# Kernel tuning notes

Hardware: AMD Instinct MI355X
Metric: run time of the kernel (lower is better)

## Reference

```python
import jax, jax.numpy as jnp
import numpy as np

DIM = 768
NUM_HEADS = 12
HEAD_DIM = DIM // NUM_HEADS
SCALE = HEAD_DIM ** (-0.5)


def setup_inputs() -> dict:
    key = jax.random.key(0)
    ks = jax.random.split(key, 8)
    B, Nq, Nk, Nv = 2, 2048, 2048, 2048
    init = 0.02
    return {
        "xq": jax.random.normal(ks[0], (B, Nq, DIM), dtype=jnp.float32),
        "xk": jax.random.normal(ks[1], (B, Nk, DIM), dtype=jnp.float32),
        "xv": jax.random.normal(ks[2], (B, Nv, DIM), dtype=jnp.float32),
        # torch nn.Linear weights are [out_features, in_features]; qkv_bias=False
        "Wq": jax.random.normal(ks[3], (DIM, DIM), dtype=jnp.float32) * init,
        "Wk": jax.random.normal(ks[4], (DIM, DIM), dtype=jnp.float32) * init,
        "Wv": jax.random.normal(ks[5], (DIM, DIM), dtype=jnp.float32) * init,
        "Wp": jax.random.normal(ks[6], (DIM, DIM), dtype=jnp.float32) * init,
        "bp": jax.random.normal(ks[7], (DIM,), dtype=jnp.float32) * init,
    }


def reference(xq, xk, xv, Wq, Wk, Wv, Wp, bp):
    B, Nq, C = xq.shape
    H, D = NUM_HEADS, HEAD_DIM
    # linear projections (torch Linear: x @ W.T), split heads -> [B, H, N, D]
    q = (xq @ Wq.T).reshape(B, Nq, H, D).transpose(0, 2, 1, 3)
    k = (xk @ Wk.T).reshape(B, xk.shape[1], H, D).transpose(0, 2, 1, 3)
    v = (xv @ Wv.T).reshape(B, xv.shape[1], H, D).transpose(0, 2, 1, 3)
    # attention scores [B, H, Nq, Nk]
    attn = jnp.einsum("bhqd,bhkd->bhqk", q, k) * SCALE
    attn = jax.nn.softmax(attn, axis=-1)
    # weighted values -> merge heads [B, Nq, C]
    out = jnp.einsum("bhqk,bhkd->bhqd", attn, v)
    out = out.transpose(0, 2, 1, 3).reshape(B, Nq, C)
    return out @ Wp.T + bp
```

## Files before the change

### kernel.cpp

```cpp
#include <hip/hip_runtime.h>
#include <hip/hip_bf16.h>


#define NSEQ 2048
#define CDIM 768
#define NH   12
#define HD   64
#define MTOT 4096
#define XEL  (MTOT*CDIM)
#define WEL  (CDIM*CDIM)
#define X8   (XEL/8)
#define W8   (WEL/8)
#define PSTR 72
#define QSCALE 0.18033688011112042f

typedef __attribute__((ext_vector_type(8))) short bf16x8;
typedef __attribute__((ext_vector_type(4))) float floatx4;

static __device__ __forceinline__ unsigned short f2bf(float f) {
  union { float f; unsigned int u; } v; v.f = f;
  return (unsigned short)((v.u + 0x8000u) >> 16);
}
static __device__ __forceinline__ unsigned pk2bf(float a, float b) {
  unsigned ua = __float_as_uint(a) + 0x8000u;
  unsigned ub = __float_as_uint(b) + 0x8000u;
  return __builtin_amdgcn_perm(ub, ua, 0x07060302);
}

static __device__ __forceinline__ void lds16(const void* g, void* l) {
  __builtin_amdgcn_global_load_lds(
      (const __attribute__((address_space(1))) unsigned int*)g,
      (__attribute__((address_space(3))) unsigned int*)l, 16, 0, 0);
}

__global__ __launch_bounds__(256) void cast_all(
    const float* __restrict__ xq, const float* __restrict__ xk,
    const float* __restrict__ xv, const float* __restrict__ wq,
    const float* __restrict__ wk, const float* __restrict__ wv,
    const float* __restrict__ wp,
    unsigned short* __restrict__ Xq, unsigned short* __restrict__ Xk,
    unsigned short* __restrict__ Xv, unsigned short* __restrict__ Wq,
    unsigned short* __restrict__ Wk, unsigned short* __restrict__ Wv,
    unsigned short* __restrict__ Wp) {
  int i = blockIdx.x * 256 + threadIdx.x;
  const float* s; unsigned short* d; int off;
  if (i < 3 * X8) {
    int t = i / X8; off = i - t * X8;
    s = (t == 0) ? xq : (t == 1) ? xk : xv;
    d = (t == 0) ? Xq : (t == 1) ? Xk : Xv;
  } else {
    int j = i - 3 * X8; int t = j / W8; off = j - t * W8;
    s = (t == 0) ? wq : (t == 1) ? wk : (t == 2) ? wv : wp;
    d = (t == 0) ? Wq : (t == 1) ? Wk : (t == 2) ? Wv : Wp;
  }
  const float4* sp = (const float4*)s + (size_t)off * 2;
  float4 a = sp[0], b = sp[1];
  uint4 o;
  o.x = pk2bf(a.x, a.y); o.y = pk2bf(a.z, a.w);
  o.z = pk2bf(b.x, b.y); o.w = pk2bf(b.z, b.w);
  *(uint4*)(d + (size_t)off * 8) = o;
}

__global__ __launch_bounds__(256) void gemm_qkv(
    const unsigned short* __restrict__ Xq, const unsigned short* __restrict__ Xk,
    const unsigned short* __restrict__ Xv, const unsigned short* __restrict__ Wq,
    const unsigned short* __restrict__ Wk, const unsigned short* __restrict__ Wv,
    unsigned short* __restrict__ Qo, unsigned short* __restrict__ Ko,
    unsigned short* __restrict__ Vo) {
  int z = blockIdx.z;
  const unsigned short* A; const unsigned short* B; int m0, n0;
  if (z == 0)      { A = Xq; B = Wq; m0 = blockIdx.y * 128; n0 = blockIdx.x * 128; }
  else if (z == 1) { A = Xk; B = Wk; m0 = blockIdx.y * 128; n0 = blockIdx.x * 128; }
  else             { A = Wv; B = Xv; m0 = blockIdx.x * 128; n0 = blockIdx.y * 128; }
  __shared__ __align__(16) unsigned short As[128 * 64];
  __shared__ __align__(16) unsigned short Bs[128 * 64];
  int tid = threadIdx.x, lane = tid & 63, wave = tid >> 6;
  int quad = lane >> 4, l15 = lane & 15, l7 = l15 & 7;
  int wm = (wave >> 1) * 64, wn = (wave & 1) * 64;
  floatx4 acc[4][4];
#pragma unroll
  for (int i = 0; i < 4; i++)
#pragma unroll
    for (int j = 0; j < 4; j++) acc[i][j] = (floatx4){0.f, 0.f, 0.f, 0.f};

  for (int k0 = 0; k0 < CDIM; k0 += 64) {
#pragma unroll
    for (int i = 0; i < 4; i++) {
      int idx = i * 256 + tid;
      int R = idx >> 3, c = (idx & 7) ^ (R & 7);
      lds16(A + (size_t)(m0 + R) * CDIM + k0 + c * 8, &As[idx * 8]);
      lds16(B + (size_t)(n0 + R) * CDIM + k0 + c * 8, &Bs[idx * 8]);
    }
    __syncthreads();
#pragma unroll
    for (int ks = 0; ks < 2; ks++) {
      int csw = ((ks * 4 + quad) ^ l7) * 8;
      bf16x8 af[4], bfr[4];
#pragma unroll
      for (int i = 0; i < 4; i++)
        af[i] = *(const bf16x8*)&As[(wm + i * 16 + l15) * 64 + csw];
#pragma unroll
      for (int i = 0; i < 4; i++)
        bfr[i] = *(const bf16x8*)&Bs[(wn + i * 16 + l15) * 64 + csw];
#pragma unroll
      for (int mi = 0; mi < 4; mi++)
#pragma unroll
        for (int ni = 0; ni < 4; ni++)
          acc[mi][ni] = __builtin_amdgcn_mfma_f32_16x16x32_bf16(
              af[mi], bfr[ni], acc[mi][ni], 0, 0, 0);
    }
    __syncthreads();
  }
#pragma unroll
  for (int mi = 0; mi < 4; mi++) {
#pragma unroll
    for (int ni = 0; ni < 4; ni++) {
#pragma unroll
      for (int r = 0; r < 4; r++) {
        int grow = m0 + wm + mi * 16 + quad * 4 + r;
        int gcol = n0 + wn + ni * 16 + l15;
        float v = acc[mi][ni][r];
        if (z == 0) {
          int b = grow >> 11, nq = grow & 2047, h = gcol >> 6, d = gcol & 63;
          Qo[((size_t)(b * NH + h) * NSEQ + nq) * HD + d] = f2bf(v * QSCALE);
        } else if (z == 1) {
          int b = grow >> 11, nq = grow & 2047, h = gcol >> 6, d = gcol & 63;
          Ko[((size_t)(b * NH + h) * NSEQ + nq) * HD + d] = f2bf(v);
        } else {
          int b = gcol >> 11, nq = gcol & 2047;
          Vo[((size_t)b * CDIM + grow) * NSEQ + nq] = f2bf(v);
        }
      }
    }
  }
}

__global__ __launch_bounds__(128) void attn_kernel(
    const unsigned short* __restrict__ Q, const unsigned short* __restrict__ K,
    const unsigned short* __restrict__ Vt, unsigned short* __restrict__ ctx) {
  int qt = blockIdx.x, bh = blockIdx.y;
  int tid = threadIdx.x, lane = tid & 63, wave = tid >> 6;
  int quad = lane >> 4, l15 = lane & 15, l7 = l15 & 7;
  __shared__ __align__(16) unsigned short Ks[2][64 * 64];
  __shared__ __align__(16) unsigned short Vs[2][64 * 64];
  __shared__ __align__(16) unsigned short Ps[2][32 * PSTR];

  const unsigned short* Qg = Q + ((size_t)bh * NSEQ + qt * 64 + wave * 32) * HD;
  const unsigned short* Kg = K + (size_t)bh * NSEQ * HD;
  const unsigned short* Vg = Vt + (size_t)bh * HD * NSEQ;

  bf16x8 qf[2][2];
#pragma unroll
  for (int qi = 0; qi < 2; qi++)
#pragma unroll
    for (int ks = 0; ks < 2; ks++)
      qf[qi][ks] = *(const bf16x8*)(Qg + (qi * 16 + l15) * HD + ks * 32 + quad * 8);

  int kgo[4], vgo[4], ldst[4];
#pragma unroll
  for (int i = 0; i < 4; i++) {
    int idx = i * 128 + tid;
    int R = idx >> 3, c = (idx & 7) ^ (R & 7);
    kgo[i] = R * HD + c * 8;
    vgo[i] = R * NSEQ + c * 8;
    ldst[i] = idx * 8;
  }
  unsigned short* Pw = &Ps[wave][0];

  float lacc[2] = {0.f, 0.f};
  floatx4 o[2][4];
#pragma unroll
  for (int qi = 0; qi < 2; qi++)
#pragma unroll
    for (int dt = 0; dt < 4; dt++) o[qi][dt] = (floatx4){0.f, 0.f, 0.f, 0.f};

  for (int tt = 0; tt < 16; tt++) {
    int k0 = tt * 128;
#pragma unroll
    for (int h = 0; h < 2; h++) {
      const unsigned short* Kh = Kg + (size_t)(k0 + h * 64) * HD;
      const unsigned short* Vh = Vg + k0 + h * 64;
#pragma unroll
      for (int i = 0; i < 4; i++) {
        lds16(Kh + kgo[i], &Ks[h][ldst[i]]);
        lds16(Vh + vgo[i], &Vs[h][ldst[i]]);
      }
    }
    __syncthreads();
#pragma unroll
    for (int h = 0; h < 2; h++) {
#pragma unroll
      for (int nt = 0; nt < 4; nt++) {
        bf16x8 kf0 = *(const bf16x8*)&Ks[h][(nt * 16 + l15) * 64 + ((quad) ^ l7) * 8];
        bf16x8 kf1 = *(const bf16x8*)&Ks[h][(nt * 16 + l15) * 64 + ((4 + quad) ^ l7) * 8];
#pragma unroll
        for (int qi = 0; qi < 2; qi++) {
          floatx4 st = (floatx4){0.f, 0.f, 0.f, 0.f};
          st = __builtin_amdgcn_mfma_f32_16x16x32_bf16(kf0, qf[qi][0], st, 0, 0, 0);
          st = __builtin_amdgcn_mfma_f32_16x16x32_bf16(kf1, qf[qi][1], st, 0, 0, 0);
          float p0 = __builtin_exp2f(st[0]), p1 = __builtin_exp2f(st[1]);
          float p2 = __builtin_exp2f(st[2]), p3 = __builtin_exp2f(st[3]);
          lacc[qi] += (p0 + p1) + (p2 + p3);
          *(uint2*)&Pw[(qi * 16 + l15) * PSTR + nt * 16 + quad * 4] =
              make_uint2(pk2bf(p0, p1), pk2bf(p2, p3));
        }
      }
#pragma unroll
      for (int ks = 0; ks < 2; ks++) {
        bf16x8 pf0 = *(const bf16x8*)&Pw[(l15) * PSTR + ks * 32 + quad * 8];
        bf16x8 pf1 = *(const bf16x8*)&Pw[(16 + l15) * PSTR + ks * 32 + quad * 8];
#pragma unroll
        for (int dt = 0; dt < 4; dt++) {
          bf16x8 vf = *(const bf16x8*)&Vs[h][(dt * 16 + l15) * 64 + ((ks * 4 + quad) ^ l7) * 8];
          o[0][dt] = __builtin_amdgcn_mfma_f32_16x16x32_bf16(vf, pf0, o[0][dt], 0, 0, 0);
          o[1][dt] = __builtin_amdgcn_mfma_f32_16x16x32_bf16(vf, pf1, o[1][dt], 0, 0, 0);
        }
      }
    }
    __syncthreads();
  }
  int b = bh / NH, h = bh - b * NH;
#pragma unroll
  for (int qi = 0; qi < 2; qi++) {
    float la = lacc[qi];
    la += __shfl_xor(la, 16, 64);
    la += __shfl_xor(la, 32, 64);
    float inv = 1.f / la;
    int qrow = qt * 64 + wave * 32 + qi * 16 + l15;
    size_t gbase = (size_t)(b * NSEQ + qrow) * CDIM + h * HD + quad * 4;
#pragma unroll
    for (int dt = 0; dt < 4; dt++) {
      float v0 = o[qi][dt][0] * inv, v1 = o[qi][dt][1] * inv;
      float v2 = o[qi][dt][2] * inv, v3 = o[qi][dt][3] * inv;
      *(uint2*)&ctx[gbase + dt * 16] = make_uint2(pk2bf(v0, v1), pk2bf(v2, v3));
    }
  }
}

__global__ __launch_bounds__(256) void gemm_out(
    const unsigned short* __restrict__ A, const unsigned short* __restrict__ B,
    const float* __restrict__ bias, float* __restrict__ out) {
  int m0 = blockIdx.y * 64, n0 = blockIdx.x * 64;
  __shared__ __align__(16) unsigned short As[64 * 64];
  __shared__ __align__(16) unsigned short Bs[64 * 64];
  int tid = threadIdx.x, lane = tid & 63, wave = tid >> 6;
  int quad = lane >> 4, l15 = lane & 15, l7 = l15 & 7;
  int wm = (wave >> 1) * 32, wn = (wave & 1) * 32;
  floatx4 acc[2][2];
#pragma unroll
  for (int i = 0; i < 2; i++)
#pragma unroll
    for (int j = 0; j < 2; j++) acc[i][j] = (floatx4){0.f, 0.f, 0.f, 0.f};

  for (int k0 = 0; k0 < CDIM; k0 += 64) {
#pragma unroll
    for (int i = 0; i < 2; i++) {
      int idx = i * 256 + tid;
      int R = idx >> 3, c = (idx & 7) ^ (R & 7);
      lds16(A + (size_t)(m0 + R) * CDIM + k0 + c * 8, &As[idx * 8]);
      lds16(B + (size_t)(n0 + R) * CDIM + k0 + c * 8, &Bs[idx * 8]);
    }
    __syncthreads();
#pragma unroll
    for (int ks = 0; ks < 2; ks++) {
      int csw = ((ks * 4 + quad) ^ l7) * 8;
      bf16x8 af[2], bfr[2];
#pragma unroll
      for (int i = 0; i < 2; i++)
        af[i] = *(const bf16x8*)&As[(wm + i * 16 + l15) * 64 + csw];
#pragma unroll
      for (int i = 0; i < 2; i++)
        bfr[i] = *(const bf16x8*)&Bs[(wn + i * 16 + l15) * 64 + csw];
#pragma unroll
      for (int mi = 0; mi < 2; mi++)
#pragma unroll
        for (int ni = 0; ni < 2; ni++)
          acc[mi][ni] = __builtin_amdgcn_mfma_f32_16x16x32_bf16(
              af[mi], bfr[ni], acc[mi][ni], 0, 0, 0);
    }
    __syncthreads();
  }
  float bv[2];
#pragma unroll
  for (int ni = 0; ni < 2; ni++) bv[ni] = bias[n0 + wn + ni * 16 + l15];
#pragma unroll
  for (int mi = 0; mi < 2; mi++)
#pragma unroll
    for (int ni = 0; ni < 2; ni++)
#pragma unroll
      for (int r = 0; r < 4; r++) {
        int grow = m0 + wm + mi * 16 + quad * 4 + r;
        int gcol = n0 + wn + ni * 16 + l15;
        out[(size_t)grow * CDIM + gcol] = acc[mi][ni][r] + bv[ni];
      }
}

extern "C" void kernel_launch(void* const* d_in, const int* in_sizes, int n_in,
                              void* d_out, int out_size, void* d_ws, size_t ws_size,
                              hipStream_t stream) {
  const float* xq = (const float*)d_in[0];
  const float* xk = (const float*)d_in[1];
  const float* xv = (const float*)d_in[2];
  const float* wq = (const float*)d_in[3];
  const float* wk = (const float*)d_in[4];
  const float* wv = (const float*)d_in[5];
  const float* wp = (const float*)d_in[6];
  const float* bp = (const float*)d_in[7];
  float* out = (float*)d_out;

  char* p = (char*)d_ws;
  unsigned short* Xq = (unsigned short*)p; p += (size_t)XEL * 2;
  unsigned short* Xk = (unsigned short*)p; p += (size_t)XEL * 2;
  unsigned short* Xv = (unsigned short*)p; p += (size_t)XEL * 2;
  unsigned short* Wq = (unsigned short*)p; p += (size_t)WEL * 2;
  unsigned short* Wk = (unsigned short*)p; p += (size_t)WEL * 2;
  unsigned short* Wv = (unsigned short*)p; p += (size_t)WEL * 2;
  unsigned short* Wp = (unsigned short*)p; p += (size_t)WEL * 2;
  unsigned short* Qb = (unsigned short*)p; p += (size_t)XEL * 2;
  unsigned short* Kb = (unsigned short*)p; p += (size_t)XEL * 2;
  unsigned short* Vb = (unsigned short*)p; p += (size_t)XEL * 2;
  unsigned short* Cx = (unsigned short*)p; p += (size_t)XEL * 2;

  cast_all<<<(3 * X8 + 4 * W8) / 256, 256, 0, stream>>>(
      xq, xk, xv, wq, wk, wv, wp, Xq, Xk, Xv, Wq, Wk, Wv, Wp);

  gemm_qkv<<<dim3(CDIM / 128, MTOT / 128, 3), 256, 0, stream>>>(
      Xq, Xk, Xv, Wq, Wk, Wv, Qb, Kb, Vb);

  attn_kernel<<<dim3(NSEQ / 64, 2 * NH), 128, 0, stream>>>(Qb, Kb, Vb, Cx);

  gemm_out<<<dim3(CDIM / 64, MTOT / 64), 256, 0, stream>>>(Cx, Wp, bp, out);
}
```

Baseline: 215.8 us.

## Double-buffer QKV GEMM LDS tiles and widen attention blocks to four waves

The QKV projection GEMM now keeps two LDS buffers per operand and prefetches the next K-slice while computing on the current one, with global offsets computed once up front. The attention kernel goes from 2 to 4 waves per block (128 query rows), so each K/V tile loaded into LDS is shared by twice as many query rows and each thread issues half as many loads. The aim is to hide global-load latency in the GEMM and to cut redundant K/V traffic in attention. The GEMM's doubled LDS use may lower occupancy. The diff does not show whether the GEMM loop keeps a barrier between prefetch and compute, so buffer reuse may be unsafe.

```diff
diff --git a/kernel.cpp b/kernel.cpp
--- a/kernel.cpp
+++ b/kernel.cpp
@@ -72,36 +72,53 @@
   if (z == 0)      { A = Xq; B = Wq; m0 = blockIdx.y * 128; n0 = blockIdx.x * 128; }
   else if (z == 1) { A = Xk; B = Wk; m0 = blockIdx.y * 128; n0 = blockIdx.x * 128; }
   else             { A = Wv; B = Xv; m0 = blockIdx.x * 128; n0 = blockIdx.y * 128; }
-  __shared__ __align__(16) unsigned short As[128 * 64];
-  __shared__ __align__(16) unsigned short Bs[128 * 64];
+  __shared__ __align__(16) unsigned short As[2][128 * 64];
+  __shared__ __align__(16) unsigned short Bs[2][128 * 64];
   int tid = threadIdx.x, lane = tid & 63, wave = tid >> 6;
   int quad = lane >> 4, l15 = lane & 15, l7 = l15 & 7;
   int wm = (wave >> 1) * 64, wn = (wave & 1) * 64;
+  int aoff[4], boff[4], lo[4];
+#pragma unroll
+  for (int i = 0; i < 4; i++) {
+    int idx = i * 256 + tid;
+    int R = idx >> 3, c = (idx & 7) ^ (R & 7);
+    aoff[i] = (m0 + R) * CDIM + c * 8;
+    boff[i] = (n0 + R) * CDIM + c * 8;
+    lo[i] = idx * 8;
+  }
   floatx4 acc[4][4];
 #pragma unroll
   for (int i = 0; i < 4; i++)
 #pragma unroll
     for (int j = 0; j < 4; j++) acc[i][j] = (floatx4){0.f, 0.f, 0.f, 0.f};
 
-  for (int k0 = 0; k0 < CDIM; k0 += 64) {
-#pragma unroll
-    for (int i = 0; i < 4; i++) {
-      int idx = i * 256 + tid;
-      int R = idx >> 3, c = (idx & 7) ^ (R & 7);
-      lds16(A + (size_t)(m0 + R) * CDIM + k0 + c * 8, &As[idx * 8]);
-      lds16(B + (size_t)(n0 + R) * CDIM + k0 + c * 8, &Bs[idx * 8]);
-    }
-    __syncthreads();
+#pragma unroll
+  for (int i = 0; i < 4; i++) {
+    lds16(A + aoff[i], &As[0][lo[i]]);
+    lds16(B + boff[i], &Bs[0][lo[i]]);
+  }
+  __syncthreads();
+
+  for (int t = 0; t < 12; t++) {
+    int cur = t & 1;
+    if (t < 11) {
+      int k1 = (t + 1) * 64;
+#pragma unroll
+      for (int i = 0; i < 4; i++) {
+        lds16(A + aoff[i] + k1, &As[cur ^ 1][lo[i]]);
+        lds16(B + boff[i] + k1, &Bs[cur ^ 1][lo[i]]);
+      }
+    }
 #pragma unroll
     for (int ks = 0; ks < 2; ks++) {
       int csw = ((ks * 4 + quad) ^ l7) * 8;
       bf16x8 af[4], bfr[4];
 #pragma unroll
       for (int i = 0; i < 4; i++)
-        af[i] = *(const bf16x8*)&As[(wm + i * 16 + l15) * 64 + csw];
+        af[i] = *(const bf16x8*)&As[cur][(wm + i * 16 + l15) * 64 + csw];
 #pragma unroll
       for (int i = 0; i < 4; i++)
-        bfr[i] = *(const bf16x8*)&Bs[(wn + i * 16 + l15) * 64 + csw];
+        bfr[i] = *(const bf16x8*)&Bs[cur][(wn + i * 16 + l15) * 64 + csw];
 #pragma unroll
       for (int mi = 0; mi < 4; mi++)
 #pragma unroll
@@ -135,7 +152,7 @@
   }
 }
 
-__global__ __launch_bounds__(128) void attn_kernel(
+__global__ __launch_bounds__(256) void attn_kernel(
     const unsigned short* __restrict__ Q, const unsigned short* __restrict__ K,
     const unsigned short* __restrict__ Vt, unsigned short* __restrict__ ctx) {
   int qt = blockIdx.x, bh = blockIdx.y;
@@ -143,9 +160,9 @@
   int quad = lane >> 4, l15 = lane & 15, l7 = l15 & 7;
   __shared__ __align__(16) unsigned short Ks[2][64 * 64];
   __shared__ __align__(16) unsigned short Vs[2][64 * 64];
-  __shared__ __align__(16) unsigned short Ps[2][32 * PSTR];
-
-  const unsigned short* Qg = Q + ((size_t)bh * NSEQ + qt * 64 + wave * 32) * HD;
+  __shared__ __align__(16) unsigned short Ps[4][32 * PSTR];
+
+  const unsigned short* Qg = Q + ((size_t)bh * NSEQ + qt * 128 + wave * 32) * HD;
   const unsigned short* Kg = K + (size_t)bh * NSEQ * HD;
   const unsigned short* Vg = Vt + (size_t)bh * HD * NSEQ;
 
@@ -156,10 +173,10 @@
     for (int ks = 0; ks < 2; ks++)
       qf[qi][ks] = *(const bf16x8*)(Qg + (qi * 16 + l15) * HD + ks * 32 + quad * 8);
 
-  int kgo[4], vgo[4], ldst[4];
-#pragma unroll
-  for (int i = 0; i < 4; i++) {
-    int idx = i * 128 + tid;
+  int kgo[2], vgo[2], ldst[2];
+#pragma unroll
+  for (int i = 0; i < 2; i++) {
+    int idx = i * 256 + tid;
     int R = idx >> 3, c = (idx & 7) ^ (R & 7);
     kgo[i] = R * HD + c * 8;
     vgo[i] = R * NSEQ + c * 8;
@@ -181,7 +198,7 @@
       const unsigned short* Kh = Kg + (size_t)(k0 + h * 64) * HD;
       const unsigned short* Vh = Vg + k0 + h * 64;
 #pragma unroll
-      for (int i = 0; i < 4; i++) {
+      for (int i = 0; i < 2; i++) {
         lds16(Kh + kgo[i], &Ks[h][ldst[i]]);
         lds16(Vh + vgo[i], &Vs[h][ldst[i]]);
       }
@@ -226,7 +243,7 @@
     la += __shfl_xor(la, 16, 64);
     la += __shfl_xor(la, 32, 64);
     float inv = 1.f / la;
-    int qrow = qt * 64 + wave * 32 + qi * 16 + l15;
+    int qrow = qt * 128 + wave * 32 + qi * 16 + l15;
     size_t gbase = (size_t)(b * NSEQ + qrow) * CDIM + h * HD + quad * 4;
 #pragma unroll
     for (int dt = 0; dt < 4; dt++) {
@@ -327,7 +344,7 @@
   gemm_qkv<<<dim3(CDIM / 128, MTOT / 128, 3), 256, 0, stream>>>(
       Xq, Xk, Xv, Wq, Wk, Wv, Qb, Kb, Vb);
 
-  attn_kernel<<<dim3(NSEQ / 64, 2 * NH), 128, 0, stream>>>(Qb, Kb, Vb, Cx);
+  attn_kernel<<<dim3(NSEQ / 128, 2 * NH), 256, 0, stream>>>(Qb, Kb, Vb, Cx);
 
   gemm_out<<<dim3(CDIM / 64, MTOT / 64), 256, 0, stream>>>(Cx, Wp, bp, out);
 }
```

After: 216.8 us. About the same (+0.4%).

## Split attention keys across wave pairs and widen out-projection K tile

Applied to the files above, without the earlier changes.

The attention kernel now runs 256 threads. Two wave-pairs each take half of the key sequence for the same 64 query rows. Their partial outputs and row sums are combined through shared memory at the end, with no max subtraction needed since exp2 is unnormalized. K/V fragments are hoisted into registers per tile. Separately, the output GEMM loads 128-wide K slices per iteration to halve the barrier count, at the cost of more LDS per block and more registers.

```diff
diff --git a/kernel.cpp b/kernel.cpp
--- a/kernel.cpp
+++ b/kernel.cpp
@@ -135,19 +135,20 @@
   }
 }
 
-__global__ __launch_bounds__(128) void attn_kernel(
+__global__ __launch_bounds__(256, 3) void attn_kernel(
     const unsigned short* __restrict__ Q, const unsigned short* __restrict__ K,
     const unsigned short* __restrict__ Vt, unsigned short* __restrict__ ctx) {
   int qt = blockIdx.x, bh = blockIdx.y;
   int tid = threadIdx.x, lane = tid & 63, wave = tid >> 6;
+  int half = wave >> 1, qsub = wave & 1;
   int quad = lane >> 4, l15 = lane & 15, l7 = l15 & 7;
   __shared__ __align__(16) unsigned short Ks[2][64 * 64];
   __shared__ __align__(16) unsigned short Vs[2][64 * 64];
-  __shared__ __align__(16) unsigned short Ps[2][32 * PSTR];
-
-  const unsigned short* Qg = Q + ((size_t)bh * NSEQ + qt * 64 + wave * 32) * HD;
-  const unsigned short* Kg = K + (size_t)bh * NSEQ * HD;
-  const unsigned short* Vg = Vt + (size_t)bh * HD * NSEQ;
+  __shared__ __align__(16) unsigned short Ps[4][16 * PSTR];
+
+  const unsigned short* Qg = Q + ((size_t)bh * NSEQ + qt * 64 + qsub * 32) * HD;
+  const unsigned short* Kg = K + ((size_t)bh * NSEQ + half * 1024) * HD;
+  const unsigned short* Vg = Vt + (size_t)bh * HD * NSEQ + half * 1024;
 
   bf16x8 qf[2][2];
 #pragma unroll
@@ -156,15 +157,18 @@
     for (int ks = 0; ks < 2; ks++)
       qf[qi][ks] = *(const bf16x8*)(Qg + (qi * 16 + l15) * HD + ks * 32 + quad * 8);
 
+  int tid2 = tid & 127;
   int kgo[4], vgo[4], ldst[4];
 #pragma unroll
   for (int i = 0; i < 4; i++) {
-    int idx = i * 128 + tid;
+    int idx = i * 128 + tid2;
     int R = idx >> 3, c = (idx & 7) ^ (R & 7);
     kgo[i] = R * HD + c * 8;
     vgo[i] = R * NSEQ + c * 8;
     ldst[i] = idx * 8;
   }
+  unsigned short* Ksh = Ks[half];
+  unsigned short* Vsh = Vs[half];
   unsigned short* Pw = &Ps[wave][0];
 
   float lacc[2] = {0.f, 0.f};
@@ -174,65 +178,81 @@
 #pragma unroll
     for (int dt = 0; dt < 4; dt++) o[qi][dt] = (floatx4){0.f, 0.f, 0.f, 0.f};
 
-  for (int tt = 0; tt < 16; tt++) {
-    int k0 = tt * 128;
-#pragma unroll
-    for (int h = 0; h < 2; h++) {
-      const unsigned short* Kh = Kg + (size_t)(k0 + h * 64) * HD;
-      const unsigned short* Vh = Vg + k0 + h * 64;
-#pragma unroll
-      for (int i = 0; i < 4; i++) {
-        lds16(Kh + kgo[i], &Ks[h][ldst[i]]);
-        lds16(Vh + vgo[i], &Vs[h][ldst[i]]);
-      }
-    }
-    __syncthreads();
-#pragma unroll
-    for (int h = 0; h < 2; h++) {
+  for (int t = 0; t < 16; t++) {
+    int k0 = t * 64;
+#pragma unroll
+    for (int i = 0; i < 4; i++) {
+      lds16(Kg + (size_t)k0 * HD + kgo[i], &Ksh[ldst[i]]);
+      lds16(Vg + k0 + vgo[i], &Vsh[ldst[i]]);
+    }
+    __syncthreads();
+    bf16x8 kf[4][2], vf[4][2];
+#pragma unroll
+    for (int nt = 0; nt < 4; nt++)
+#pragma unroll
+      for (int x = 0; x < 2; x++)
+        kf[nt][x] = *(const bf16x8*)&Ksh[(nt * 16 + l15) * 64 + ((x * 4 + quad) ^ l7) * 8];
+#pragma unroll
+    for (int dt = 0; dt < 4; dt++)
+#pragma unroll
+      for (int x = 0; x < 2; x++)
+        vf[dt][x] = *(const bf16x8*)&Vs[half][(dt * 16 + l15) * 64 + ((x * 4 + quad) ^ l7) * 8];
+#pragma unroll
+    for (int qi = 0; qi < 2; qi++) {
 #pragma unroll
       for (int nt = 0; nt < 4; nt++) {
-        bf16x8 kf0 = *(const bf16x8*)&Ks[h][(nt * 16 + l15) * 64 + ((quad) ^ l7) * 8];
-        bf16x8 kf1 = *(const bf16x8*)&Ks[h][(nt * 16 + l15) * 64 + ((4 + quad) ^ l7) * 8];
-#pragma unroll
-        for (int qi = 0; qi < 2; qi++) {
-          floatx4 st = (floatx4){0.f, 0.f, 0.f, 0.f};
-          st = __builtin_amdgcn_mfma_f32_16x16x32_bf16(kf0, qf[qi][0], st, 0, 0, 0);
-          st = __builtin_amdgcn_mfma_f32_16x16x32_bf16(kf1, qf[qi][1], st, 0, 0, 0);
-          float p0 = __builtin_exp2f(st[0]), p1 = __builtin_exp2f(st[1]);
-          float p2 = __builtin_exp2f(st[2]), p3 = __builtin_exp2f(st[3]);
-          lacc[qi] += (p0 + p1) + (p2 + p3);
-          *(uint2*)&Pw[(qi * 16 + l15) * PSTR + nt * 16 + quad * 4] =
-              make_uint2(pk2bf(p0, p1), pk2bf(p2, p3));
-        }
+        floatx4 st = (floatx4){0.f, 0.f, 0.f, 0.f};
+        st = __builtin_amdgcn_mfma_f32_16x16x32_bf16(kf[nt][0], qf[qi][0], st, 0, 0, 0);
+        st = __builtin_amdgcn_mfma_f32_16x16x32_bf16(kf[nt][1], qf[qi][1], st, 0, 0, 0);
+        float p0 = __builtin_exp2f(st[0]), p1 = __builtin_exp2f(st[1]);
+        float p2 = __builtin_exp2f(st[2]), p3 = __builtin_exp2f(st[3]);
+        lacc[qi] += (p0 + p1) + (p2 + p3);
+        *(uint2*)&Pw[l15 * PSTR + nt * 16 + quad * 4] =
+            make_uint2(pk2bf(p0, p1), pk2bf(p2, p3));
       }
 #pragma unroll
       for (int ks = 0; ks < 2; ks++) {
-        bf16x8 pf0 = *(const bf16x8*)&Pw[(l15) * PSTR + ks * 32 + quad * 8];
-        bf16x8 pf1 = *(const bf16x8*)&Pw[(16 + l15) * PSTR + ks * 32 + quad * 8];
-#pragma unroll
-        for (int dt = 0; dt < 4; dt++) {
-          bf16x8 vf = *(const bf16x8*)&Vs[h][(dt * 16 + l15) * 64 + ((ks * 4 + quad) ^ l7) * 8];
-          o[0][dt] = __builtin_amdgcn_mfma_f32_16x16x32_bf16(vf, pf0, o[0][dt], 0, 0, 0);
-          o[1][dt] = __builtin_amdgcn_mfma_f32_16x16x32_bf16(vf, pf1, o[1][dt], 0, 0, 0);
-        }
-      }
-    }
-    __syncthreads();
-  }
-  int b = bh / NH, h = bh - b * NH;
+        bf16x8 pf = *(const bf16x8*)&Pw[l15 * PSTR + ks * 32 + quad * 8];
+#pragma unroll
+        for (int dt = 0; dt < 4; dt++)
+          o[qi][dt] = __builtin_amdgcn_mfma_f32_16x16x32_bf16(vf[dt][ks], pf, o[qi][dt], 0, 0, 0);
+      }
+    }
+    __syncthreads();
+  }
 #pragma unroll
   for (int qi = 0; qi < 2; qi++) {
-    float la = lacc[qi];
-    la += __shfl_xor(la, 16, 64);
-    la += __shfl_xor(la, 32, 64);
-    float inv = 1.f / la;
-    int qrow = qt * 64 + wave * 32 + qi * 16 + l15;
-    size_t gbase = (size_t)(b * NSEQ + qrow) * CDIM + h * HD + quad * 4;
-#pragma unroll
-    for (int dt = 0; dt < 4; dt++) {
-      float v0 = o[qi][dt][0] * inv, v1 = o[qi][dt][1] * inv;
-      float v2 = o[qi][dt][2] * inv, v3 = o[qi][dt][3] * inv;
-      *(uint2*)&ctx[gbase + dt * 16] = make_uint2(pk2bf(v0, v1), pk2bf(v2, v3));
+    lacc[qi] += __shfl_xor(lacc[qi], 16, 64);
+    lacc[qi] += __shfl_xor(lacc[qi], 32, 64);
+  }
+  float* Obuf = (float*)&Ks[0][0];
+  float* Lbuf = (float*)&Ps[0][0];
+  if (half == 1) {
+#pragma unroll
+    for (int qi = 0; qi < 2; qi++) {
+      int ro = qsub * 32 + qi * 16 + l15;
+#pragma unroll
+      for (int dt = 0; dt < 4; dt++)
+        *(floatx4*)&Obuf[ro * 64 + dt * 16 + quad * 4] = o[qi][dt];
+      if (quad == 0) Lbuf[ro] = lacc[qi];
+    }
+  }
+  __syncthreads();
+  if (half == 0) {
+    int b = bh / NH, h = bh - b * NH;
+#pragma unroll
+    for (int qi = 0; qi < 2; qi++) {
+      int ro = qsub * 32 + qi * 16 + l15;
+      float inv = 1.f / (lacc[qi] + Lbuf[ro]);
+      int qrow = qt * 64 + ro;
+      size_t gbase = (size_t)(b * NSEQ + qrow) * CDIM + h * HD + quad * 4;
+#pragma unroll
+      for (int dt = 0; dt < 4; dt++) {
+        floatx4 ob = *(floatx4*)&Obuf[ro * 64 + dt * 16 + quad * 4];
+        float v0 = (o[qi][dt][0] + ob[0]) * inv, v1 = (o[qi][dt][1] + ob[1]) * inv;
+        float v2 = (o[qi][dt][2] + ob[2]) * inv, v3 = (o[qi][dt][3] + ob[3]) * inv;
+        *(uint2*)&ctx[gbase + dt * 16] = make_uint2(pk2bf(v0, v1), pk2bf(v2, v3));
+      }
     }
   }
 }
@@ -241,8 +261,8 @@
     const unsigned short* __restrict__ A, const unsigned short* __restrict__ B,
     const float* __restrict__ bias, float* __restrict__ out) {
   int m0 = blockIdx.y * 64, n0 = blockIdx.x * 64;
-  __shared__ __align__(16) unsigned short As[64 * 64];
-  __shared__ __align__(16) unsigned short Bs[64 * 64];
+  __shared__ __align__(16) unsigned short As[64 * 128];
+  __shared__ __align__(16) unsigned short Bs[64 * 128];
   int tid = threadIdx.x, lane = tid & 63, wave = tid >> 6;
   int quad = lane >> 4, l15 = lane & 15, l7 = l15 & 7;
   int wm = (wave >> 1) * 32, wn = (wave & 1) * 32;
@@ -252,25 +272,27 @@
 #pragma unroll
     for (int j = 0; j < 2; j++) acc[i][j] = (floatx4){0.f, 0.f, 0.f, 0.f};
 
-  for (int k0 = 0; k0 < CDIM; k0 += 64) {
-#pragma unroll
-    for (int i = 0; i < 2; i++) {
+  for (int k0 = 0; k0 < CDIM; k0 += 128) {
+#pragma unroll
+    for (int i = 0; i < 4; i++) {
       int idx = i * 256 + tid;
-      int R = idx >> 3, c = (idx & 7) ^ (R & 7);
-      lds16(A + (size_t)(m0 + R) * CDIM + k0 + c * 8, &As[idx * 8]);
-      lds16(B + (size_t)(n0 + R) * CDIM + k0 + c * 8, &Bs[idx * 8]);
-    }
-    __syncthreads();
-#pragma unroll
-    for (int ks = 0; ks < 2; ks++) {
-      int csw = ((ks * 4 + quad) ^ l7) * 8;
+      int R = idx >> 4, c4 = idx & 15;
+      int cs = (c4 & 8) | ((c4 & 7) ^ (R & 7));
+      lds16(A + (size_t)(m0 + R) * CDIM + k0 + cs * 8, &As[idx * 8]);
+      lds16(B + (size_t)(n0 + R) * CDIM + k0 + cs * 8, &Bs[idx * 8]);
+    }
+    __syncthreads();
+#pragma unroll
+    for (int ks = 0; ks < 4; ks++) {
+      int c = ks * 4 + quad;
+      int csw = ((c & 8) | ((c & 7) ^ l7)) * 8;
       bf16x8 af[2], bfr[2];
 #pragma unroll
       for (int i = 0; i < 2; i++)
-        af[i] = *(const bf16x8*)&As[(wm + i * 16 + l15) * 64 + csw];
+        af[i] = *(const bf16x8*)&As[(wm + i * 16 + l15) * 128 + csw];
 #pragma unroll
       for (int i = 0; i < 2; i++)
-        bfr[i] = *(const bf16x8*)&Bs[(wn + i * 16 + l15) * 64 + csw];
+        bfr[i] = *(const bf16x8*)&Bs[(wn + i * 16 + l15) * 128 + csw];
 #pragma unroll
       for (int mi = 0; mi < 2; mi++)
 #pragma unroll
@@ -327,7 +349,7 @@
   gemm_qkv<<<dim3(CDIM / 128, MTOT / 128, 3), 256, 0, stream>>>(
       Xq, Xk, Xv, Wq, Wk, Wv, Qb, Kb, Vb);
 
-  attn_kernel<<<dim3(NSEQ / 64, 2 * NH), 128, 0, stream>>>(Qb, Kb, Vb, Cx);
+  attn_kernel<<<dim3(NSEQ / 64, 2 * NH), 256, 0, stream>>>(Qb, Kb, Vb, Cx);
 
   gemm_out<<<dim3(CDIM / 64, MTOT / 64), 256, 0, stream>>>(Cx, Wp, bp, out);
 }
```

Result: faster. 201.4 us (-6.7%).
